# Kernel optimization log

Measured on AMD Instinct MI355X. Metric: run time of the kernel, lower is better.

The kernel has to match this reference:

```python
import jax, jax.numpy as jnp
import numpy as np

D = 64
H = 8


def setup_inputs() -> dict:
    key = jax.random.key(0)
    ks = jax.random.split(key, 6)
    b, l = 2, 4096
    scale = 1.0 / np.sqrt(D)
    x = jax.random.normal(ks[0], (b, l, D), dtype=jnp.float32)
    Wq = jax.random.normal(ks[1], (D, D * H), dtype=jnp.float32) * scale
    Wk = jax.random.normal(ks[2], (D, D * H), dtype=jnp.float32) * scale
    Wv = jax.random.normal(ks[3], (D, D * H), dtype=jnp.float32) * scale
    Wu = jax.random.normal(ks[4], (H * D, D), dtype=jnp.float32) * (1.0 / np.sqrt(H * D))
    bu = jax.random.normal(ks[5], (D,), dtype=jnp.float32) * 0.01
    return {"x": x, "Wq": Wq, "Wk": Wk, "Wv": Wv, "Wu": Wu, "bu": bu}


def reference(x, Wq, Wk, Wv, Wu, bu):
    b, l, d = x.shape
    h = H
    # per-head projections: each head uses FULL width d (as in the torch module)
    q = jnp.einsum('bld,de->ble', x, Wq).reshape(b, l, h, d)
    k = jnp.einsum('bld,de->ble', x, Wk).reshape(b, l, h, d)
    v = jnp.einsum('bld,de->ble', x, Wv).reshape(b, l, h, d)
    # scores [b,h,l,l] scaled by 1/sqrt(d)
    scores = jnp.einsum('blhd,bmhd->bhlm', q, k) / jnp.sqrt(jnp.asarray(d, x.dtype))
    w = jax.nn.softmax(scores, axis=-1)
    out = jnp.einsum('bhlm,bmhd->blhd', w, v).reshape(b, l, h * d)
    return out @ Wu + bu
```

## Files before the change

kernel.cpp:

```cpp
#include <hip/hip_runtime.h>
#include <hip/hip_bf16.h>
#include <stdint.h>

typedef float  f32x16 __attribute__((ext_vector_type(16)));
typedef __bf16 bf16x8 __attribute__((ext_vector_type(8)));

#define WS_QG    0
#define WS_KG    8388608
#define WS_VTG   16777216
#define WS_ATTN  25165824
#define WS_WT    33554432
#define WS_WUT   33751040

__device__ __forceinline__ f32x16 zero16(){
  f32x16 z;
  #pragma unroll
  for (int i = 0; i < 16; ++i) z[i] = 0.0f;
  return z;
}

__device__ __forceinline__ uint16_t bf16b(float v){
  return __builtin_bit_cast(uint16_t, __float2bfloat16(v));
}

__device__ __forceinline__ uint32_t pk2(float a, float b){
  return (uint32_t)bf16b(a) | ((uint32_t)bf16b(b) << 16);
}

__device__ __forceinline__ void plswap(uint32_t &a, uint32_t &b){
  asm volatile("v_permlane32_swap_b32 %0, %1" : "+v"(a), "+v"(b));
}

__global__ void prep_w(const float* __restrict__ Wq, const float* __restrict__ Wk,
                       const float* __restrict__ Wv, const float* __restrict__ Wu,
                       char* __restrict__ ws){
  int tid = blockIdx.x * 256 + threadIdx.x;
  if (tid < 3*32768){
    int which = tid >> 15;
    int idx   = tid & 32767;
    int e = idx & 511, k = idx >> 9;
    const float* W = (which == 0) ? Wq : (which == 1 ? Wk : Wv);
    float v = W[k*512 + e];
    if (which == 0) v *= 0.18033688011112042f;
    ((uint16_t*)(ws + WS_WT))[which*32768 + e*64 + k] = bf16b(v);
  } else {
    int idx = tid - 3*32768;
    int c = idx & 63, e = idx >> 6;
    ((uint16_t*)(ws + WS_WUT))[c*512 + e] = bf16b(Wu[e*64 + c]);
  }
}

__global__ __launch_bounds__(256,2) void qkv_proj(const float* __restrict__ x,
                                                  char* __restrict__ ws){
  const int lane = threadIdx.x & 63;
  const int wid  = blockIdx.x*4 + (threadIdx.x >> 6);
  const int rt   = wid / 24;
  const int rem  = wid % 24;
  const int mm   = rem >> 3, cb = rem & 7;
  const int col  = lane & 31, hi = lane >> 5;

  const uint16_t* Wt = (const uint16_t*)(ws + WS_WT) + mm*32768;

  bf16x8 af[4];
  {
    const float* xr = x + (size_t)(rt*32 + col)*64 + hi*8;
    #pragma unroll
    for (int ks = 0; ks < 4; ++ks){
      float4 a0 = *(const float4*)(xr + ks*16);
      float4 a1 = *(const float4*)(xr + ks*16 + 4);
      uint4 u;
      u.x = pk2(a0.x, a0.y); u.y = pk2(a0.z, a0.w);
      u.z = pk2(a1.x, a1.y); u.w = pk2(a1.z, a1.w);
      af[ks] = __builtin_bit_cast(bf16x8, u);
    }
  }

  f32x16 acc0 = zero16(), acc1 = zero16();
  {
    const uint16_t* w0p = Wt + (size_t)(cb*64 + col)*64 + hi*8;
    const uint16_t* w1p = w0p + 32*64;
    #pragma unroll
    for (int ks = 0; ks < 4; ++ks){
      bf16x8 b0 = *(const bf16x8*)(w0p + ks*16);
      bf16x8 b1 = *(const bf16x8*)(w1p + ks*16);
      acc0 = __builtin_amdgcn_mfma_f32_32x32x16_bf16(af[ks], b0, acc0, 0, 0, 0);
      acc1 = __builtin_amdgcn_mfma_f32_32x32x16_bf16(af[ks], b1, acc1, 0, 0, 0);
    }
  }

  uint16_t* Qg  = (uint16_t*)(ws + WS_QG);
  uint16_t* Kg  = (uint16_t*)(ws + WS_KG);
  uint16_t* Vtg = (uint16_t*)(ws + WS_VTG);
  #pragma unroll
  for (int r = 0; r < 16; ++r){
    int row  = rt*32 + (r&3) + 8*(r>>2) + 4*hi;
    int b    = row >> 12, ltok = row & 4095;
    uint16_t v0 = bf16b(acc0[r]), v1 = bf16b(acc1[r]);
    if (mm == 2){
      Vtg[(size_t)((b*8 + cb)*64 + col     )*4096 + ltok] = v0;
      Vtg[(size_t)((b*8 + cb)*64 + col + 32)*4096 + ltok] = v1;
    } else {
      uint16_t* G = mm ? Kg : Qg;
      size_t base = (size_t)((b*8 + cb)*4096 + ltok)*64;
      G[base + col]      = v0;
      G[base + col + 32] = v1;
    }
  }
}

__global__ __launch_bounds__(256,2) void attn_fa(char* __restrict__ ws){
  const int lane = threadIdx.x & 63;
  const int wave = threadIdx.x >> 6;
  const int qt   = blockIdx.x & 31;
  const int bh   = blockIdx.x >> 5;
  const int col  = lane & 31, hi = lane >> 5;

  const uint16_t* Qg  = (const uint16_t*)(ws + WS_QG)  + (size_t)bh*262144;
  const uint16_t* Kg  = (const uint16_t*)(ws + WS_KG)  + (size_t)bh*262144;
  const uint16_t* Vtg = (const uint16_t*)(ws + WS_VTG) + (size_t)bh*262144;
  uint16_t* attn = (uint16_t*)(ws + WS_ATTN);

  __shared__ __align__(16) char smem[50176];
  char* kb0 = smem;
  char* kb1 = smem + 4096;
  char* vb0 = smem + 8192;
  char* vb1 = smem + 12288;
  float* otl = (float*)(smem + 16384);

  const int qbase = qt*128 + wave*32;

  bf16x8 qf[4];
  {
    const uint16_t* qr = Qg + (size_t)(qbase + col)*64 + hi*8;
    #pragma unroll
    for (int ds = 0; ds < 4; ++ds) qf[ds] = *(const bf16x8*)(qr + ds*16);
  }

  const int kr = wave*8  + (lane >> 3), kj = lane & 7;
  const int vr = wave*16 + (lane >> 2), vj = lane & 3;
  const int kDst = (kr*128 + kj*16) ^ ((kr & 7) << 4);
  const int vDst = (vr*64  + vj*16) ^ ((vr & 3) << 4);
  const uint16_t* kSrcBase = Kg  + (size_t)kr*64  + kj*8;
  const uint16_t* vSrcBase = Vtg + (size_t)vr*4096 + vj*8;

  f32x16 ot0 = zero16(), ot1 = zero16();
  float mrun = -1e30f, lrun = 0.0f;

  {
    uint4 k0 = *(const uint4*)(kSrcBase);
    uint4 v0 = *(const uint4*)(vSrcBase);
    *(uint4*)(kb0 + kDst) = k0;
    *(uint4*)(vb0 + vDst) = v0;
  }
  __syncthreads();

  uint4 kreg, vreg;
  for (int t = 0; t < 128; ++t){
    const bool last = (t == 127);
    if (!last){
      kreg = *(const uint4*)(kSrcBase + (size_t)(t+1)*2048);
      vreg = *(const uint4*)(vSrcBase + (size_t)(t+1)*32);
    }
    const char* kb = (t & 1) ? kb1 : kb0;
    const char* vb = (t & 1) ? vb1 : vb0;

    f32x16 s = zero16();
    #pragma unroll
    for (int ds = 0; ds < 4; ++ds){
      bf16x8 kf = *(const bf16x8*)(kb + ((col*128 + hi*16 + ds*32) ^ ((col & 7) << 4)));
      s = __builtin_amdgcn_mfma_f32_32x32x16_bf16(kf, qf[ds], s, 0, 0, 0);
    }

    float tmax = s[0];
    #pragma unroll
    for (int r = 1; r < 16; ++r) tmax = fmaxf(tmax, s[r]);
    tmax = fmaxf(tmax, __shfl_xor(tmax, 32));
    const bool skip = __all(tmax <= mrun) != 0;
    float mnew = skip ? mrun : fmaxf(mrun, tmax);
    float p[16];
    #pragma unroll
    for (int r = 0; r < 16; ++r) p[r] = __builtin_amdgcn_exp2f(s[r] - mnew);
    float rs = 0.0f;
    #pragma unroll
    for (int r = 0; r < 16; ++r) rs += p[r];
    rs += __shfl_xor(rs, 32);
    if (!skip){
      float al = __builtin_amdgcn_exp2f(mrun - mnew);
      lrun = lrun * al + rs;
      mrun = mnew;
      #pragma unroll
      for (int r = 0; r < 16; ++r){ ot0[r] *= al; ot1[r] *= al; }
    } else {
      lrun += rs;
    }

    uint32_t w0 = pk2(p[0],  p[1]),  w1 = pk2(p[2],  p[3]);
    uint32_t w2 = pk2(p[4],  p[5]),  w3 = pk2(p[6],  p[7]);
    uint32_t w4 = pk2(p[8],  p[9]),  w5 = pk2(p[10], p[11]);
    uint32_t w6 = pk2(p[12], p[13]), w7 = pk2(p[14], p[15]);
    plswap(w0, w2); plswap(w1, w3); plswap(w4, w6); plswap(w5, w7);
    uint4 u0; u0.x = w0; u0.y = w1; u0.z = w2; u0.w = w3;
    uint4 u1; u1.x = w4; u1.y = w5; u1.z = w6; u1.w = w7;
    bf16x8 pf0 = __builtin_bit_cast(bf16x8, u0);
    bf16x8 pf1 = __builtin_bit_cast(bf16x8, u1);

    {
      bf16x8 vf;
      vf  = *(const bf16x8*)(vb + ((col*64 + hi*16     ) ^ ((col & 3) << 4)));
      ot0 = __builtin_amdgcn_mfma_f32_32x32x16_bf16(vf, pf0, ot0, 0, 0, 0);
      vf  = *(const bf16x8*)(vb + ((col*64 + hi*16 + 32) ^ ((col & 3) << 4)));
      ot0 = __builtin_amdgcn_mfma_f32_32x32x16_bf16(vf, pf1, ot0, 0, 0, 0);
      const int dv1 = col + 32;
      vf  = *(const bf16x8*)(vb + ((dv1*64 + hi*16     ) ^ ((dv1 & 3) << 4)));
      ot1 = __builtin_amdgcn_mfma_f32_32x32x16_bf16(vf, pf0, ot1, 0, 0, 0);
      vf  = *(const bf16x8*)(vb + ((dv1*64 + hi*16 + 32) ^ ((dv1 & 3) << 4)));
      ot1 = __builtin_amdgcn_mfma_f32_32x32x16_bf16(vf, pf1, ot1, 0, 0, 0);
    }

    if (!last){
      char* kbn = (t & 1) ? kb0 : kb1;
      char* vbn = (t & 1) ? vb0 : vb1;
      *(uint4*)(kbn + kDst) = kreg;
      *(uint4*)(vbn + vDst) = vreg;
    }
    __syncthreads();
  }

  float inv = 1.0f / lrun;
  #pragma unroll
  for (int r = 0; r < 16; ++r){ ot0[r] *= inv; ot1[r] *= inv; }

  float* ow = otl + wave*2112;
  #pragma unroll
  for (int r = 0; r < 16; ++r){
    int dv = (r&3) + 8*(r>>2) + 4*hi;
    ow[dv*33 + col]        = ot0[r];
    ow[(dv + 32)*33 + col] = ot1[r];
  }
  __syncthreads();

  {
    int tq = threadIdx.x >> 1, dh = threadIdx.x & 1;
    const float* orow = otl + (tq >> 5)*2112 + (tq & 31);
    int token = (bh >> 3)*4096 + qt*128 + tq;
    uint16_t* arow = attn + (size_t)token*512 + (bh & 7)*64 + dh*32;
    #pragma unroll
    for (int j4 = 0; j4 < 4; ++j4){
      int dd = dh*32 + j4*8;
      uint4 u;
      u.x = pk2(orow[(dd+0)*33], orow[(dd+1)*33]);
      u.y = pk2(orow[(dd+2)*33], orow[(dd+3)*33]);
      u.z = pk2(orow[(dd+4)*33], orow[(dd+5)*33]);
      u.w = pk2(orow[(dd+6)*33], orow[(dd+7)*33]);
      *(uint4*)(arow + j4*8) = u;
    }
  }
}

__global__ __launch_bounds__(256,2) void out_proj(const char* __restrict__ ws,
                                                  const float* __restrict__ bu,
                                                  float* __restrict__ out){
  const int lane = threadIdx.x & 63;
  const int col  = lane & 31, hi = lane >> 5;
  const int rt   = blockIdx.x*4 + (threadIdx.x >> 6);

  const uint16_t* attn = (const uint16_t*)(ws + WS_ATTN);
  const uint16_t* Wut  = (const uint16_t*)(ws + WS_WUT);

  f32x16 a0 = zero16(), a1 = zero16();
  const uint16_t* ar  = attn + (size_t)(rt*32 + col)*512 + hi*8;
  const uint16_t* b0p = Wut + (size_t)col*512 + hi*8;
  const uint16_t* b1p = b0p + 32*512;
  #pragma unroll 8
  for (int ks = 0; ks < 32; ++ks){
    bf16x8 af = *(const bf16x8*)(ar  + ks*16);
    bf16x8 b0 = *(const bf16x8*)(b0p + ks*16);
    bf16x8 b1 = *(const bf16x8*)(b1p + ks*16);
    a0 = __builtin_amdgcn_mfma_f32_32x32x16_bf16(af, b0, a0, 0, 0, 0);
    a1 = __builtin_amdgcn_mfma_f32_32x32x16_bf16(af, b1, a1, 0, 0, 0);
  }
  float bias0 = bu[col], bias1 = bu[col + 32];
  #pragma unroll
  for (int r = 0; r < 16; ++r){
    int row = rt*32 + (r&3) + 8*(r>>2) + 4*hi;
    out[(size_t)row*64 + col]      = a0[r] + bias0;
    out[(size_t)row*64 + col + 32] = a1[r] + bias1;
  }
}

extern "C" void kernel_launch(void* const* d_in, const int* in_sizes, int n_in,
                              void* d_out, int out_size, void* d_ws, size_t ws_size,
                              hipStream_t stream){
  const float* x  = (const float*)d_in[0];
  const float* Wq = (const float*)d_in[1];
  const float* Wk = (const float*)d_in[2];
  const float* Wv = (const float*)d_in[3];
  const float* Wu = (const float*)d_in[4];
  const float* bu = (const float*)d_in[5];
  char*  ws  = (char*)d_ws;
  float* out = (float*)d_out;

  prep_w  <<<dim3(512),  dim3(256), 0, stream>>>(Wq, Wk, Wv, Wu, ws);
  qkv_proj<<<dim3(1536), dim3(256), 0, stream>>>(x, ws);
  attn_fa <<<dim3(512),  dim3(256), 0, stream>>>(ws);
  out_proj<<<dim3(64),   dim3(256), 0, stream>>>(ws, bu, out);
}
```

Baseline: 222.8 us.

## Restructure attention into single-wave blocks with unrolled double-buffered K/V pipeline

The attention kernel is rewritten so each 64-thread block handles one 32-query tile and loads full 32-key K/V tiles itself. This removes the per-iteration block-wide barriers and uses a two-deep register prefetch with LDS ping-pong plus s_setprio around the MFMAs. The V transpose store in qkv_proj is staged through LDS to produce coalesced 16-byte writes. out_proj switches to 16x16x32 MFMA tiles across 512 blocks to increase parallelism. Single-wave blocks lose K/V sharing across waves, so global/L2 traffic for K and V rises roughly fourfold.

```diff
diff --git a/kernel.cpp b/kernel.cpp
--- a/kernel.cpp
+++ b/kernel.cpp
@@ -3,6 +3,7 @@
 #include <stdint.h>
 
 typedef float  f32x16 __attribute__((ext_vector_type(16)));
+typedef float  f32x4  __attribute__((ext_vector_type(4)));
 typedef __bf16 bf16x8 __attribute__((ext_vector_type(8)));
 
 #define WS_QG    0
@@ -53,11 +54,14 @@
 __global__ __launch_bounds__(256,2) void qkv_proj(const float* __restrict__ x,
                                                   char* __restrict__ ws){
   const int lane = threadIdx.x & 63;
-  const int wid  = blockIdx.x*4 + (threadIdx.x >> 6);
+  const int widx = threadIdx.x >> 6;
+  const int wid  = blockIdx.x*4 + widx;
   const int rt   = wid / 24;
   const int rem  = wid % 24;
   const int mm   = rem >> 3, cb = rem & 7;
   const int col  = lane & 31, hi = lane >> 5;
+
+  __shared__ __align__(16) uint16_t tbuf[4][64*40];
 
   const uint16_t* Wt = (const uint16_t*)(ws + WS_WT) + mm*32768;
 
@@ -91,28 +95,40 @@
   uint16_t* Qg  = (uint16_t*)(ws + WS_QG);
   uint16_t* Kg  = (uint16_t*)(ws + WS_KG);
   uint16_t* Vtg = (uint16_t*)(ws + WS_VTG);
-  #pragma unroll
-  for (int r = 0; r < 16; ++r){
-    int row  = rt*32 + (r&3) + 8*(r>>2) + 4*hi;
-    int b    = row >> 12, ltok = row & 4095;
-    uint16_t v0 = bf16b(acc0[r]), v1 = bf16b(acc1[r]);
-    if (mm == 2){
-      Vtg[(size_t)((b*8 + cb)*64 + col     )*4096 + ltok] = v0;
-      Vtg[(size_t)((b*8 + cb)*64 + col + 32)*4096 + ltok] = v1;
-    } else {
-      uint16_t* G = mm ? Kg : Qg;
+  if (mm == 2){
+    uint16_t* tb = tbuf[widx];
+    #pragma unroll
+    for (int r = 0; r < 16; ++r){
+      int tok = (r&3) + 8*(r>>2) + 4*hi;
+      tb[col*40 + tok]        = bf16b(acc0[r]);
+      tb[(col+32)*40 + tok]   = bf16b(acc1[r]);
+    }
+    int b    = (rt*32) >> 12;
+    int ltok = (rt*32) & 4095;
+    const int vrow = lane >> 2, ch = lane & 3;
+    #pragma unroll
+    for (int o = 0; o < 4; ++o){
+      int dv = o*16 + vrow;
+      uint4 u = *(const uint4*)(tb + dv*40 + ch*8);
+      *(uint4*)(Vtg + ((size_t)((b*8 + cb)*64 + dv))*4096 + ltok + ch*8) = u;
+    }
+  } else {
+    uint16_t* G = mm ? Kg : Qg;
+    #pragma unroll
+    for (int r = 0; r < 16; ++r){
+      int row  = rt*32 + (r&3) + 8*(r>>2) + 4*hi;
+      int b    = row >> 12, ltok = row & 4095;
       size_t base = (size_t)((b*8 + cb)*4096 + ltok)*64;
-      G[base + col]      = v0;
-      G[base + col + 32] = v1;
-    }
-  }
-}
-
-__global__ __launch_bounds__(256,2) void attn_fa(char* __restrict__ ws){
-  const int lane = threadIdx.x & 63;
-  const int wave = threadIdx.x >> 6;
-  const int qt   = blockIdx.x & 31;
-  const int bh   = blockIdx.x >> 5;
+      G[base + col]      = bf16b(acc0[r]);
+      G[base + col + 32] = bf16b(acc1[r]);
+    }
+  }
+}
+
+__global__ __launch_bounds__(64) void attn_fa(char* __restrict__ ws){
+  const int lane = threadIdx.x;
+  const int qt   = blockIdx.x & 127;
+  const int bh   = blockIdx.x >> 7;
   const int col  = lane & 31, hi = lane >> 5;
 
   const uint16_t* Qg  = (const uint16_t*)(ws + WS_QG)  + (size_t)bh*262144;
@@ -120,14 +136,13 @@
   const uint16_t* Vtg = (const uint16_t*)(ws + WS_VTG) + (size_t)bh*262144;
   uint16_t* attn = (uint16_t*)(ws + WS_ATTN);
 
-  __shared__ __align__(16) char smem[50176];
+  __shared__ __align__(16) char smem[18432];
   char* kb0 = smem;
   char* kb1 = smem + 4096;
   char* vb0 = smem + 8192;
-  char* vb1 = smem + 12288;
-  float* otl = (float*)(smem + 16384);
-
-  const int qbase = qt*128 + wave*32;
+  char* vb1 = smem + 13312;
+
+  const int qbase = qt*32;
 
   bf16x8 qf[4];
   {
@@ -136,53 +151,57 @@
     for (int ds = 0; ds < 4; ++ds) qf[ds] = *(const bf16x8*)(qr + ds*16);
   }
 
-  const int kr = wave*8  + (lane >> 3), kj = lane & 7;
-  const int vr = wave*16 + (lane >> 2), vj = lane & 3;
-  const int kDst = (kr*128 + kj*16) ^ ((kr & 7) << 4);
-  const int vDst = (vr*64  + vj*16) ^ ((vr & 3) << 4);
-  const uint16_t* kSrcBase = Kg  + (size_t)kr*64  + kj*8;
-  const uint16_t* vSrcBase = Vtg + (size_t)vr*4096 + vj*8;
+  const int krow = lane >> 3, kj = lane & 7;
+  const int vrow = lane >> 2, vj = lane & 3;
+  const uint16_t* kSrc = Kg  + (size_t)krow*64   + kj*8;
+  const uint16_t* vSrc = Vtg + (size_t)vrow*4096 + vj*8;
+  const int kDst = (krow*128 + kj*16) ^ (krow << 4);
+  const int vDst = vrow*80 + vj*16;
 
   f32x16 ot0 = zero16(), ot1 = zero16();
   float mrun = -1e30f, lrun = 0.0f;
 
-  {
-    uint4 k0 = *(const uint4*)(kSrcBase);
-    uint4 v0 = *(const uint4*)(vSrcBase);
-    *(uint4*)(kb0 + kDst) = k0;
-    *(uint4*)(vb0 + vDst) = v0;
-  }
-  __syncthreads();
-
-  uint4 kreg, vreg;
-  for (int t = 0; t < 128; ++t){
-    const bool last = (t == 127);
-    if (!last){
-      kreg = *(const uint4*)(kSrcBase + (size_t)(t+1)*2048);
-      vreg = *(const uint4*)(vSrcBase + (size_t)(t+1)*32);
-    }
-    const char* kb = (t & 1) ? kb1 : kb0;
-    const char* vb = (t & 1) ? vb1 : vb0;
-
+  auto loadK = [&](uint4* r, int t){
+    const uint16_t* s = kSrc + (size_t)t*2048;
+    #pragma unroll
+    for (int o = 0; o < 4; ++o) r[o] = *(const uint4*)(s + o*512);
+  };
+  auto loadV = [&](uint4* r, int t){
+    const uint16_t* s = vSrc + t*32;
+    #pragma unroll
+    for (int o = 0; o < 4; ++o) r[o] = *(const uint4*)(s + (size_t)o*65536);
+  };
+  auto writeKV = [&](char* kb, char* vb, const uint4* kr, const uint4* vr){
+    #pragma unroll
+    for (int o = 0; o < 4; ++o) *(uint4*)(kb + kDst + o*1024) = kr[o];
+    #pragma unroll
+    for (int o = 0; o < 4; ++o) *(uint4*)(vb + vDst + o*1280) = vr[o];
+  };
+
+  auto compute = [&](const char* kb, const char* vb){
     f32x16 s = zero16();
+    __builtin_amdgcn_s_setprio(1);
     #pragma unroll
     for (int ds = 0; ds < 4; ++ds){
       bf16x8 kf = *(const bf16x8*)(kb + ((col*128 + hi*16 + ds*32) ^ ((col & 7) << 4)));
       s = __builtin_amdgcn_mfma_f32_32x32x16_bf16(kf, qf[ds], s, 0, 0, 0);
     }
-
-    float tmax = s[0];
-    #pragma unroll
-    for (int r = 1; r < 16; ++r) tmax = fmaxf(tmax, s[r]);
+    __builtin_amdgcn_s_setprio(0);
+
+    float t0 = fmaxf(fmaxf(s[0],  s[1]),  fmaxf(s[2],  s[3]));
+    float t1 = fmaxf(fmaxf(s[4],  s[5]),  fmaxf(s[6],  s[7]));
+    float t2 = fmaxf(fmaxf(s[8],  s[9]),  fmaxf(s[10], s[11]));
+    float t3 = fmaxf(fmaxf(s[12], s[13]), fmaxf(s[14], s[15]));
+    float tmax = fmaxf(fmaxf(t0, t1), fmaxf(t2, t3));
     tmax = fmaxf(tmax, __shfl_xor(tmax, 32));
     const bool skip = __all(tmax <= mrun) != 0;
     float mnew = skip ? mrun : fmaxf(mrun, tmax);
     float p[16];
     #pragma unroll
     for (int r = 0; r < 16; ++r) p[r] = __builtin_amdgcn_exp2f(s[r] - mnew);
-    float rs = 0.0f;
-    #pragma unroll
-    for (int r = 0; r < 16; ++r) rs += p[r];
+    float a0 = (p[0]+p[1]) + (p[2]+p[3]),   a1 = (p[4]+p[5]) + (p[6]+p[7]);
+    float a2 = (p[8]+p[9]) + (p[10]+p[11]), a3 = (p[12]+p[13]) + (p[14]+p[15]);
+    float rs = (a0 + a1) + (a2 + a3);
     rs += __shfl_xor(rs, 32);
     if (!skip){
       float al = __builtin_amdgcn_exp2f(mrun - mnew);
@@ -204,87 +223,94 @@
     bf16x8 pf0 = __builtin_bit_cast(bf16x8, u0);
     bf16x8 pf1 = __builtin_bit_cast(bf16x8, u1);
 
+    __builtin_amdgcn_s_setprio(1);
     {
       bf16x8 vf;
-      vf  = *(const bf16x8*)(vb + ((col*64 + hi*16     ) ^ ((col & 3) << 4)));
+      vf  = *(const bf16x8*)(vb + col*80 + hi*16);
       ot0 = __builtin_amdgcn_mfma_f32_32x32x16_bf16(vf, pf0, ot0, 0, 0, 0);
-      vf  = *(const bf16x8*)(vb + ((col*64 + hi*16 + 32) ^ ((col & 3) << 4)));
+      vf  = *(const bf16x8*)(vb + col*80 + hi*16 + 32);
       ot0 = __builtin_amdgcn_mfma_f32_32x32x16_bf16(vf, pf1, ot0, 0, 0, 0);
-      const int dv1 = col + 32;
-      vf  = *(const bf16x8*)(vb + ((dv1*64 + hi*16     ) ^ ((dv1 & 3) << 4)));
+      vf  = *(const bf16x8*)(vb + (col+32)*80 + hi*16);
       ot1 = __builtin_amdgcn_mfma_f32_32x32x16_bf16(vf, pf0, ot1, 0, 0, 0);
-      vf  = *(const bf16x8*)(vb + ((dv1*64 + hi*16 + 32) ^ ((dv1 & 3) << 4)));
+      vf  = *(const bf16x8*)(vb + (col+32)*80 + hi*16 + 32);
       ot1 = __builtin_amdgcn_mfma_f32_32x32x16_bf16(vf, pf1, ot1, 0, 0, 0);
     }
-
-    if (!last){
-      char* kbn = (t & 1) ? kb0 : kb1;
-      char* vbn = (t & 1) ? vb0 : vb1;
-      *(uint4*)(kbn + kDst) = kreg;
-      *(uint4*)(vbn + vDst) = vreg;
-    }
-    __syncthreads();
-  }
+    __builtin_amdgcn_s_setprio(0);
+  };
+
+  uint4 kA[4], vA[4], kB[4], vB[4];
+  loadK(kA, 0); loadV(vA, 0);
+  writeKV(kb0, vb0, kA, vA);
+  loadK(kA, 1); loadV(vA, 1);
+
+  for (int t = 0; t < 126; t += 2){
+    loadK(kB, t+2); loadV(vB, t+2);
+    compute(kb0, vb0);
+    writeKV(kb1, vb1, kA, vA);
+    loadK(kA, t+3); loadV(vA, t+3);
+    compute(kb1, vb1);
+    writeKV(kb0, vb0, kB, vB);
+  }
+  compute(kb0, vb0);
+  writeKV(kb1, vb1, kA, vA);
+  compute(kb1, vb1);
 
   float inv = 1.0f / lrun;
   #pragma unroll
   for (int r = 0; r < 16; ++r){ ot0[r] *= inv; ot1[r] *= inv; }
 
-  float* ow = otl + wave*2112;
+  uint16_t* owb = (uint16_t*)smem;
   #pragma unroll
   for (int r = 0; r < 16; ++r){
     int dv = (r&3) + 8*(r>>2) + 4*hi;
-    ow[dv*33 + col]        = ot0[r];
-    ow[(dv + 32)*33 + col] = ot1[r];
-  }
-  __syncthreads();
-
+    owb[dv*33 + col]        = bf16b(ot0[r]);
+    owb[(dv + 32)*33 + col] = bf16b(ot1[r]);
+  }
   {
-    int tq = threadIdx.x >> 1, dh = threadIdx.x & 1;
-    const float* orow = otl + (tq >> 5)*2112 + (tq & 31);
-    int token = (bh >> 3)*4096 + qt*128 + tq;
-    uint16_t* arow = attn + (size_t)token*512 + (bh & 7)*64 + dh*32;
-    #pragma unroll
-    for (int j4 = 0; j4 < 4; ++j4){
-      int dd = dh*32 + j4*8;
-      uint4 u;
-      u.x = pk2(orow[(dd+0)*33], orow[(dd+1)*33]);
-      u.y = pk2(orow[(dd+2)*33], orow[(dd+3)*33]);
-      u.z = pk2(orow[(dd+4)*33], orow[(dd+5)*33]);
-      u.w = pk2(orow[(dd+6)*33], orow[(dd+7)*33]);
-      *(uint4*)(arow + j4*8) = u;
-    }
-  }
-}
-
-__global__ __launch_bounds__(256,2) void out_proj(const char* __restrict__ ws,
-                                                  const float* __restrict__ bu,
-                                                  float* __restrict__ out){
+    const int ch = lane & 7;
+    #pragma unroll
+    for (int o = 0; o < 4; ++o){
+      int tok = o*8 + (lane >> 3);
+      uint32_t wv[4];
+      #pragma unroll
+      for (int jj = 0; jj < 4; ++jj){
+        uint32_t lo = owb[(ch*8 + jj*2    )*33 + tok];
+        uint32_t hh = owb[(ch*8 + jj*2 + 1)*33 + tok];
+        wv[jj] = lo | (hh << 16);
+      }
+      uint4 u; u.x = wv[0]; u.y = wv[1]; u.z = wv[2]; u.w = wv[3];
+      size_t row = (size_t)((bh >> 3)*4096 + qbase + tok);
+      *(uint4*)(attn + row*512 + (bh & 7)*64 + ch*8) = u;
+    }
+  }
+}
+
+__global__ __launch_bounds__(256) void out_proj(const char* __restrict__ ws,
+                                                const float* __restrict__ bu,
+                                                float* __restrict__ out){
   const int lane = threadIdx.x & 63;
-  const int col  = lane & 31, hi = lane >> 5;
-  const int rt   = blockIdx.x*4 + (threadIdx.x >> 6);
+  const int wave = blockIdx.x*4 + (threadIdx.x >> 6);
+  const int mt = wave >> 2, cb = wave & 3;
+  const int rc = lane & 15, kg = lane >> 4;
 
   const uint16_t* attn = (const uint16_t*)(ws + WS_ATTN);
   const uint16_t* Wut  = (const uint16_t*)(ws + WS_WUT);
 
-  f32x16 a0 = zero16(), a1 = zero16();
-  const uint16_t* ar  = attn + (size_t)(rt*32 + col)*512 + hi*8;
-  const uint16_t* b0p = Wut + (size_t)col*512 + hi*8;
-  const uint16_t* b1p = b0p + 32*512;
-  #pragma unroll 8
-  for (int ks = 0; ks < 32; ++ks){
-    bf16x8 af = *(const bf16x8*)(ar  + ks*16);
-    bf16x8 b0 = *(const bf16x8*)(b0p + ks*16);
-    bf16x8 b1 = *(const bf16x8*)(b1p + ks*16);
-    a0 = __builtin_amdgcn_mfma_f32_32x32x16_bf16(af, b0, a0, 0, 0, 0);
-    a1 = __builtin_amdgcn_mfma_f32_32x32x16_bf16(af, b1, a1, 0, 0, 0);
-  }
-  float bias0 = bu[col], bias1 = bu[col + 32];
-  #pragma unroll
-  for (int r = 0; r < 16; ++r){
-    int row = rt*32 + (r&3) + 8*(r>>2) + 4*hi;
-    out[(size_t)row*64 + col]      = a0[r] + bias0;
-    out[(size_t)row*64 + col + 32] = a1[r] + bias1;
+  const uint16_t* ar = attn + (size_t)(mt*16 + rc)*512 + kg*8;
+  const uint16_t* bp = Wut  + (size_t)(cb*16 + rc)*512 + kg*8;
+
+  f32x4 acc = {0.0f, 0.0f, 0.0f, 0.0f};
+  #pragma unroll
+  for (int ks = 0; ks < 16; ++ks){
+    bf16x8 af = *(const bf16x8*)(ar + ks*32);
+    bf16x8 bf = *(const bf16x8*)(bp + ks*32);
+    acc = __builtin_amdgcn_mfma_f32_16x16x32_bf16(af, bf, acc, 0, 0, 0);
+  }
+  float bias = bu[cb*16 + rc];
+  #pragma unroll
+  for (int r = 0; r < 4; ++r){
+    int orow = mt*16 + kg*4 + r;
+    out[(size_t)orow*64 + cb*16 + rc] = acc[r] + bias;
   }
 }
 
@@ -302,6 +328,6 @@
 
   prep_w  <<<dim3(512),  dim3(256), 0, stream>>>(Wq, Wk, Wv, Wu, ws);
   qkv_proj<<<dim3(1536), dim3(256), 0, stream>>>(x, ws);
-  attn_fa <<<dim3(512),  dim3(256), 0, stream>>>(ws);
-  out_proj<<<dim3(64),   dim3(256), 0, stream>>>(ws, bu, out);
-}
+  attn_fa <<<dim3(2048), dim3(64),  0, stream>>>(ws);
+  out_proj<<<dim3(512),  dim3(256), 0, stream>>>(ws, bu, out);
+}
```

Result: slower. 639.6 us (+187.1%).
